# Kernel optimization log

Hardware: AMD Instinct MI355X
Metric: run time of the kernel (lower is better)

Reference implementation:

```python
import jax, jax.numpy as jnp
import numpy as np

D_MODEL, D_STATE, D_CONV, EXPAND = 1024, 16, 4, 2
D_INNER = EXPAND * D_MODEL          # 2048
DT_RANK = D_MODEL // 16             # 64
B, L = 2, 1024


def setup_inputs() -> dict:
    key = jax.random.key(0)
    ks = jax.random.split(key, 10)
    x = jax.random.normal(ks[0], (B, L, D_MODEL), dtype=jnp.float32)
    ln_w = jnp.ones((D_MODEL,), jnp.float32)
    ln_b = jnp.zeros((D_MODEL,), jnp.float32)
    in_proj_w = jax.random.normal(ks[1], (2 * D_INNER, D_MODEL), jnp.float32) * (D_MODEL ** -0.5)
    conv_w = jax.random.normal(ks[2], (D_INNER, 1, D_CONV), jnp.float32) * (D_CONV ** -0.5)
    conv_b = jnp.zeros((D_INNER,), jnp.float32)
    x_proj_w = jax.random.normal(ks[3], (DT_RANK + 2 * D_STATE, D_INNER), jnp.float32) * (D_INNER ** -0.5)
    dt_proj_w = jax.random.normal(ks[4], (D_INNER, DT_RANK), jnp.float32) * (DT_RANK ** -0.5)
    # dt bias: inverse-softplus of dt sampled log-uniform in [1e-3, 1e-1] (mamba init)
    dt = jnp.exp(jax.random.uniform(ks[5], (D_INNER,)) * (np.log(0.1) - np.log(1e-3)) + np.log(1e-3))
    dt_proj_b = dt + jnp.log(-jnp.expm1(-dt))
    # A_log: log of [1..d_state] repeated per channel (S4D-real init)
    A_log = jnp.log(jnp.broadcast_to(jnp.arange(1, D_STATE + 1, dtype=jnp.float32), (D_INNER, D_STATE)))
    D = jnp.ones((D_INNER,), jnp.float32)
    out_proj_w = jax.random.normal(ks[6], (D_MODEL, D_INNER), jnp.float32) * (D_INNER ** -0.5)
    return dict(x=x, ln_w=ln_w, ln_b=ln_b, in_proj_w=in_proj_w, conv_w=conv_w,
                conv_b=conv_b, x_proj_w=x_proj_w, dt_proj_w=dt_proj_w,
                dt_proj_b=dt_proj_b, A_log=A_log, D=D, out_proj_w=out_proj_w)


def _layernorm(x, w, b, eps=1e-5):
    mu = jnp.mean(x, axis=-1, keepdims=True)
    var = jnp.mean(jnp.square(x - mu), axis=-1, keepdims=True)
    return (x - mu) * jax.lax.rsqrt(var + eps) * w + b


def _mamba(h, in_proj_w, conv_w, conv_b, x_proj_w, dt_proj_w, dt_proj_b, A_log, D, out_proj_w):
    # h: (B, L, d_model)
    xz = jnp.einsum('bld,ed->ble', h, in_proj_w)          # (B,L,2*d_inner)
    x_in, z = jnp.split(xz, 2, axis=-1)                   # each (B,L,d_inner)
    # depthwise causal conv1d
    kernel = jnp.transpose(conv_w, (2, 1, 0))             # (d_conv, 1, d_inner) LIO
    x_conv = jax.lax.conv_general_dilated(
        x_in, kernel, window_strides=(1,), padding=[(D_CONV - 1, 0)],
        dimension_numbers=('NLC', 'LIO', 'NLC'), feature_group_count=D_INNER)
    x_conv = jax.nn.silu(x_conv + conv_b)                 # (B,L,d_inner)
    # input-dependent SSM parameters
    x_dbl = jnp.einsum('bld,ed->ble', x_conv, x_proj_w)   # (B,L,dt_rank+2*d_state)
    dt, B_ssm, C_ssm = jnp.split(x_dbl, [DT_RANK, DT_RANK + D_STATE], axis=-1)
    dt = jax.nn.softplus(jnp.einsum('blr,dr->bld', dt, dt_proj_w) + dt_proj_b)  # (B,L,d_inner)
    A = -jnp.exp(A_log)                                   # (d_inner, d_state)
    deltaA = jnp.exp(dt[..., None] * A)                   # (B,L,d_inner,d_state)
    deltaBu = dt[..., None] * B_ssm[:, :, None, :] * x_conv[..., None]
    # selective scan: h_t = deltaA_t * h_{t-1} + deltaBu_t (parallel associative scan over L)
    def combine(left, right):
        a_l, b_l = left
        a_r, b_r = right
        return a_l * a_r, b_l * a_r + b_r
    _, states = jax.lax.associative_scan(combine, (deltaA, deltaBu), axis=1)
    y = jnp.einsum('blds,bls->bld', states, C_ssm) + x_conv * D
    y = y * jax.nn.silu(z)
    return jnp.einsum('bld,ed->ble', y, out_proj_w)       # (B,L,d_model)


def reference(x, ln_w, ln_b, in_proj_w, conv_w, conv_b, x_proj_w, dt_proj_w,
              dt_proj_b, A_log, D, out_proj_w):
    h = _layernorm(x, ln_w, ln_b)
    return x + _mamba(h, in_proj_w, conv_w, conv_b, x_proj_w, dt_proj_w,
                      dt_proj_b, A_log, D, out_proj_w)
```

## Files before the change

kernel.cpp:

```cpp
#include <hip/hip_runtime.h>
#include <hip/hip_bf16.h>
#include <math.h>

#define DM   1024
#define DI   2048
#define DS   16
#define DTR  64
#define NB   2
#define LL   1024
#define MR   (NB*LL)
#define XDBL 96
#define NC   32
#define CL   32

typedef _Float16 half8  __attribute__((ext_vector_type(8)));
typedef _Float16 half4v __attribute__((ext_vector_type(4)));
typedef float    floatx4 __attribute__((ext_vector_type(4)));

__device__ __forceinline__ void gload_lds16(const void* g, void* l) {
  __builtin_amdgcn_global_load_lds(
      (const __attribute__((address_space(1))) void*)g,
      (__attribute__((address_space(3))) void*)l, 16, 0, 0);
}

__global__ __launch_bounds__(256) void front_kernel(
    const float* __restrict__ x, const float* __restrict__ ln_w,
    const float* __restrict__ ln_b,
    const float* __restrict__ w_in, const float* __restrict__ w_out,
    const float* __restrict__ w_xp, const float* __restrict__ w_dt,
    _Float16* __restrict__ h_h,
    _Float16* __restrict__ w_in_h, _Float16* __restrict__ w_out_h,
    _Float16* __restrict__ w_xp_h, _Float16* __restrict__ w_dt_h) {
  const int blk = blockIdx.x;
  if (blk < MR) {
    __shared__ float sA[4], sB[4];
    const float* xr = x + (size_t)blk * DM;
    float s = 0.f, ss = 0.f;
    for (int i = threadIdx.x; i < DM; i += 256) {
      float v = xr[i];
      s += v; ss += v * v;
    }
    for (int o = 32; o > 0; o >>= 1) {
      s  += __shfl_down(s, o, 64);
      ss += __shfl_down(ss, o, 64);
    }
    const int wid = threadIdx.x >> 6, lid = threadIdx.x & 63;
    if (lid == 0) { sA[wid] = s; sB[wid] = ss; }
    __syncthreads();
    if (threadIdx.x == 0) {
      float S = sA[0] + sA[1] + sA[2] + sA[3];
      float SS = sB[0] + sB[1] + sB[2] + sB[3];
      float mu = S / DM;
      sA[0] = mu;
      sB[0] = rsqrtf(SS / DM - mu * mu + 1e-5f);
    }
    __syncthreads();
    const float mu = sA[0], rs = sB[0];
    for (int i = threadIdx.x; i < DM; i += 256)
      h_h[(size_t)blk * DM + i] = (_Float16)((xr[i] - mu) * rs * ln_w[i] + ln_b[i]);
    return;
  }
  int i = (blk - MR) * 256 + threadIdx.x;
  const int N0 = 1048576, N1 = 524288, N2 = 49152, N3 = 32768;
  const float* s; _Float16* d; int off;
  if (i < N0)            { s = w_in;  d = w_in_h;  off = i; }
  else if (i < N0+N1)    { s = w_out; d = w_out_h; off = i - N0; }
  else if (i < N0+N1+N2) { s = w_xp;  d = w_xp_h;  off = i - N0 - N1; }
  else if (i < N0+N1+N2+N3) { s = w_dt; d = w_dt_h; off = i - N0 - N1 - N2; }
  else return;
  float4 v = ((const float4*)s)[off];
  half4v h = {(_Float16)v.x, (_Float16)v.y, (_Float16)v.z, (_Float16)v.w};
  ((half4v*)d)[off] = h;
}

template <int EPI, int TN, int KS>
__global__ __launch_bounds__(256) void gemm_mfma(
    const _Float16* __restrict__ A,
    const _Float16* __restrict__ W,
    void* __restrict__ Cv, void* __restrict__ C2v,
    const float* __restrict__ extra, int ldc,
    int M, int N, int K, int kchunk) {
  constexpr int NT = (TN + 31) / 32;
  constexpr int WSLOT = TN / 16;
  constexpr int SLAB = 32 * KS;
  __shared__ alignas(16) _Float16 As[2][128 * 32 * KS];
  __shared__ alignas(16) _Float16 Ws[2][TN * 32 * KS];
  const int t = threadIdx.x;
  const int wave = t >> 6, lane = t & 63;
  const int m0 = blockIdx.y * 128, n0 = blockIdx.x * TN;
  const int k_beg = blockIdx.z * kchunk;
  const int nk = kchunk / SLAB;
  const int wm = (wave >> 1) * 64, wn = (wave & 1) * (TN / 2);
  floatx4 acc[4][NT];
#pragma unroll
  for (int i = 0; i < 4; i++)
#pragma unroll
    for (int j = 0; j < NT; j++) acc[i][j] = {0.f, 0.f, 0.f, 0.f};

  const int fr = lane & 15;
  const int kc8 = lane >> 4;
  const int kp = (kc8 ^ ((fr >> 1) & 3)) * 8;

  auto stage = [&](int buf, int k0) {
    for (int sl = wave; sl < 8 * KS; sl += 4) {
      const int ss = sl >> 3, s8 = sl & 7;
      const int idx = s8 * 64 + lane;
      const int row = idx >> 2;
      const int kc = (idx & 3) ^ ((row >> 1) & 3);
      gload_lds16(A + (size_t)(m0 + row) * K + k0 + ss * 32 + kc * 8,
                  &As[buf][ss * 4096 + s8 * 512]);
    }
    for (int sl = wave; sl < WSLOT * KS; sl += 4) {
      const int ss = sl / WSLOT, sw = sl % WSLOT;
      const int idx = sw * 64 + lane;
      const int row = idx >> 2;
      const int kc = (idx & 3) ^ ((row >> 1) & 3);
      const int wrow = (n0 + row < N) ? row : 0;
      gload_lds16(W + (size_t)(n0 + wrow) * K + k0 + ss * 32 + kc * 8,
                  &Ws[buf][ss * (TN * 32) + sw * 512]);
    }
  };

  stage(0, k_beg);
  int cur = 0;
  for (int ki = 0; ki < nk; ki++) {
    __syncthreads();
    if (ki + 1 < nk) stage(cur ^ 1, k_beg + (ki + 1) * SLAB);
#pragma unroll
    for (int ks = 0; ks < KS; ks++) {
      half8 af[4], wf[NT];
#pragma unroll
      for (int i = 0; i < 4; i++)
        af[i] = *(const half8*)&As[cur][ks * 4096 + (wm + i * 16 + fr) * 32 + kp];
#pragma unroll
      for (int j = 0; j < NT; j++)
        wf[j] = *(const half8*)&Ws[cur][ks * (TN * 32) + (wn + j * 16 + fr) * 32 + kp];
#pragma unroll
      for (int i = 0; i < 4; i++)
#pragma unroll
        for (int j = 0; j < NT; j++)
          acc[i][j] = __builtin_amdgcn_mfma_f32_16x16x32_f16(af[i], wf[j], acc[i][j], 0, 0, 0);
    }
    cur ^= 1;
  }

  const int col = lane & 15, rowq = lane >> 4;
#pragma unroll
  for (int i = 0; i < 4; i++) {
#pragma unroll
    for (int j = 0; j < NT; j++) {
      const int n = n0 + wn + j * 16 + col;
      if (n < N) {
#pragma unroll
        for (int r = 0; r < 4; r++) {
          const int m = m0 + wm + i * 16 + rowq * 4 + r;
          float v = acc[i][j][r];
          if (EPI == 0) {
            if (n < DI) ((_Float16*)Cv )[(size_t)m * DI + n]      = (_Float16)v;
            else        ((_Float16*)C2v)[(size_t)m * DI + n - DI] = (_Float16)v;
          } else if (EPI == 4) {
            ((_Float16*)Cv)[((size_t)blockIdx.z * M + m) * ldc + n] = (_Float16)v;
          } else if (EPI == 5) {
            v += extra[n];
            v = (v > 20.f) ? v : __logf(1.f + __expf(v));
            ((_Float16*)Cv)[(size_t)m * ldc + n] = (_Float16)v;
          }
        }
      }
    }
  }
}

__global__ __launch_bounds__(256) void xproj_reduce(
    const _Float16* __restrict__ part,
    float* __restrict__ x_dbl, _Float16* __restrict__ dtr) {
  const int idx = blockIdx.x * 256 + threadIdx.x;
  const int m = idx / XDBL, c = idx - m * XDBL;
  float s = 0.f;
#pragma unroll
  for (int z = 0; z < 16; z++) s += (float)part[(size_t)z * (MR * XDBL) + idx];
  x_dbl[idx] = s;
  if (c < DTR) dtr[m * DTR + c] = (_Float16)s;
}

__global__ __launch_bounds__(256) void out_reduce(
    const float* __restrict__ x, const _Float16* __restrict__ part,
    float* __restrict__ out) {
  const int i = blockIdx.x * 256 + threadIdx.x;
  float4 a = ((const float4*)x)[i];
#pragma unroll
  for (int z = 0; z < 4; z++) {
    half4v p = ((const half4v*)(part + (size_t)z * MR * DM))[i];
    a.x += (float)p.x; a.y += (float)p.y; a.z += (float)p.z; a.w += (float)p.w;
  }
  ((float4*)out)[i] = a;
}

__global__ __launch_bounds__(256) void conv_silu_kernel(
    const _Float16* __restrict__ xin, const float* __restrict__ cw,
    const float* __restrict__ cb, _Float16* __restrict__ xc) {
  const int idx = blockIdx.x * 256 + threadIdx.x;
  const int d8 = idx & (DI / 8 - 1);
  const int ml = idx >> 8;
  const int l  = ml & (LL - 1);
  const int d0 = d8 * 8;
  half8 xr[4];
  const half8 zero = {0, 0, 0, 0, 0, 0, 0, 0};
#pragma unroll
  for (int k = 0; k < 4; k++) {
    const int lp = l - 3 + k;
    xr[k] = (lp >= 0) ? *(const half8*)&xin[(size_t)(ml - 3 + k) * DI + d0] : zero;
  }
  half8 o;
#pragma unroll
  for (int j = 0; j < 8; j++) {
    float acc = cb[d0 + j];
#pragma unroll
    for (int k = 0; k < 4; k++)
      acc += (float)xr[k][j] * cw[(d0 + j) * 4 + k];
    o[j] = (_Float16)(acc / (1.f + __expf(-acc)));
  }
  *(half8*)&xc[(size_t)ml * DI + d0] = o;
}

__device__ __forceinline__ bool load_a(const float* __restrict__ A_log, int d,
                                       float* a) {
  const float4* Ap = (const float4*)(A_log + (size_t)d * DS);
  bool fast = true;
#pragma unroll
  for (int i = 0; i < 4; i++) {
    float4 v = Ap[i];
    a[4 * i + 0] = -__expf(v.x); a[4 * i + 1] = -__expf(v.y);
    a[4 * i + 2] = -__expf(v.z); a[4 * i + 3] = -__expf(v.w);
  }
#pragma unroll
  for (int s = 0; s < DS; s++)
    fast = fast && (fabsf(a[s] + (float)(s + 1)) < 1e-4f);
  return fast;
}

__global__ __launch_bounds__(256) void scan_phase1(
    const _Float16* __restrict__ xc,
    const float* __restrict__ xdbl,
    const _Float16* __restrict__ dtm,
    const float* __restrict__ A_log,
    float* __restrict__ HE,
    float* __restrict__ SA) {
  __shared__ float Bs[CL][DS];
  const int bi = blockIdx.x;
  const int dblk = bi & 7;
  const int c = (bi >> 3) & (NC - 1);
  const int b = bi >> 8;
  const int t = threadIdx.x;
  const int d = dblk * 256 + t;
  const int mlbase = b * LL + c * CL;

  for (int i = t; i < CL * DS; i += 256) {
    int tt = i >> 4, s = i & 15;
    Bs[tt][s] = xdbl[(size_t)(mlbase + tt) * XDBL + DTR + s];
  }

  float a[DS];
  const bool fast = load_a(A_log, d, a);
  float h[DS];
#pragma unroll
  for (int s = 0; s < DS; s++) h[s] = 0.f;
  float S = 0.f;
  __syncthreads();

  if (fast) {
    for (int tt = 0; tt < CL; tt++) {
      const size_t ml = mlbase + tt;
      const float dtv = (float)dtm[ml * DI + d];
      const float u   = (float)xc[ml * DI + d];
      const float du  = dtv * u;
      S += dtv;
      const float r = __expf(-dtv);
      float P = 1.f;
#pragma unroll
      for (int s = 0; s < DS; s++) {
        P *= r;
        h[s] = P * h[s] + du * Bs[tt][s];
      }
    }
  } else {
    for (int tt = 0; tt < CL; tt++) {
      const size_t ml = mlbase + tt;
      const float dtv = (float)dtm[ml * DI + d];
      const float u   = (float)xc[ml * DI + d];
      const float du  = dtv * u;
      S += dtv;
#pragma unroll
      for (int s = 0; s < DS; s++)
        h[s] = __expf(dtv * a[s]) * h[s] + du * Bs[tt][s];
    }
  }
  const size_t base = ((size_t)(b * NC + c) * DS) * DI + d;
#pragma unroll
  for (int s = 0; s < DS; s++) HE[base + (size_t)s * DI] = h[s];
  SA[(size_t)(b * NC + c) * DI + d] = S;
}

__global__ __launch_bounds__(256) void scan_phase2(
    const float* __restrict__ A_log,
    const float* __restrict__ SA,
    float* __restrict__ HE) {
  const int idx = blockIdx.x * 256 + threadIdx.x;
  const int d = idx & (DI - 1);
  const int s = (idx >> 11) & (DS - 1);
  const int b = idx >> 15;
  const float a = -__expf(A_log[(size_t)d * DS + s]);
  float Hc = 0.f;
  for (int c = 0; c < NC; c++) {
    const size_t o = ((size_t)(b * NC + c) * DS + s) * DI + d;
    const float he = HE[o];
    const float P = __expf(a * SA[(size_t)(b * NC + c) * DI + d]);
    HE[o] = Hc;
    Hc = P * Hc + he;
  }
}

__global__ __launch_bounds__(256) void scan_phase3(
    const _Float16* __restrict__ xc,
    const float* __restrict__ xdbl,
    const _Float16* __restrict__ dtm,
    const _Float16* __restrict__ zbuf,
    const float* __restrict__ A_log,
    const float* __restrict__ Dvec,
    const float* __restrict__ HE,
    _Float16* __restrict__ y) {
  __shared__ float Bs[CL][DS];
  __shared__ float Cs[CL][DS];
  const int bi = blockIdx.x;
  const int dblk = bi & 7;
  const int c = (bi >> 3) & (NC - 1);
  const int b = bi >> 8;
  const int t = threadIdx.x;
  const int d = dblk * 256 + t;
  const int mlbase = b * LL + c * CL;

  for (int i = t; i < CL * DS; i += 256) {
    int tt = i >> 4, s = i & 15;
    const size_t ro = (size_t)(mlbase + tt) * XDBL + DTR + s;
    Bs[tt][s] = xdbl[ro];
    Cs[tt][s] = xdbl[ro + DS];
  }

  float a[DS];
  const bool fast = load_a(A_log, d, a);
  float h[DS];
  const size_t base = ((size_t)(b * NC + c) * DS) * DI + d;
#pragma unroll
  for (int s = 0; s < DS; s++) h[s] = HE[base + (size_t)s * DI];
  const float Dv = Dvec[d];
  __syncthreads();

  if (fast) {
    for (int tt = 0; tt < CL; tt++) {
      const size_t ml = mlbase + tt;
      const float dtv = (float)dtm[ml * DI + d];
      const float u   = (float)xc[ml * DI + d];
      const float du  = dtv * u;
      const float r = __expf(-dtv);
      float P = 1.f, p = 0.f;
#pragma unroll
      for (int s = 0; s < DS; s++) {
        P *= r;
        h[s] = P * h[s] + du * Bs[tt][s];
        p += h[s] * Cs[tt][s];
      }
      const float zv = (float)zbuf[ml * DI + d];
      const float sil = zv / (1.f + __expf(-zv));
      y[ml * DI + d] = (_Float16)((p + u * Dv) * sil);
    }
  } else {
    for (int tt = 0; tt < CL; tt++) {
      const size_t ml = mlbase + tt;
      const float dtv = (float)dtm[ml * DI + d];
      const float u   = (float)xc[ml * DI + d];
      const float du  = dtv * u;
      float p = 0.f;
#pragma unroll
      for (int s = 0; s < DS; s++) {
        h[s] = __expf(dtv * a[s]) * h[s] + du * Bs[tt][s];
        p += h[s] * Cs[tt][s];
      }
      const float zv = (float)zbuf[ml * DI + d];
      const float sil = zv / (1.f + __expf(-zv));
      y[ml * DI + d] = (_Float16)((p + u * Dv) * sil);
    }
  }
}

extern "C" void kernel_launch(void* const* d_in, const int* in_sizes, int n_in,
                              void* d_out, int out_size, void* d_ws, size_t ws_size,
                              hipStream_t stream) {
  const float* x         = (const float*)d_in[0];
  const float* ln_w      = (const float*)d_in[1];
  const float* ln_b      = (const float*)d_in[2];
  const float* in_proj_w = (const float*)d_in[3];
  const float* conv_w    = (const float*)d_in[4];
  const float* conv_b    = (const float*)d_in[5];
  const float* x_proj_w  = (const float*)d_in[6];
  const float* dt_proj_w = (const float*)d_in[7];
  const float* dt_proj_b = (const float*)d_in[8];
  const float* A_log     = (const float*)d_in[9];
  const float* Dvec      = (const float*)d_in[10];
  const float* out_proj_w= (const float*)d_in[11];
  float* out = (float*)d_out;

  char* ws = (char*)d_ws;
  _Float16* h_h      = (_Float16*)ws;
  _Float16* xin_h    = (_Float16*)(ws + 4194304);
  _Float16* y_h      = xin_h;
  _Float16* z_h      = (_Float16*)(ws + 12582912);
  _Float16* xc_h     = (_Float16*)(ws + 20971520);
  _Float16* dtb_h    = (_Float16*)(ws + 29360128);
  _Float16* out_part = dtb_h;
  float*    x_dbl    = (float*)   (ws + 46137344);
  float*    SA       = (float*)   (ws + 46923776);
  _Float16* dtr_h    = (_Float16*)(ws + 47448064);
  float*    HE       = (float*)   (ws + 47710208);
  _Float16* w_in_h   = (_Float16*)(ws + 56098816);
  _Float16* w_out_h  = (_Float16*)(ws + 64487424);
  _Float16* w_xp_h   = (_Float16*)(ws + 68681728);
  _Float16* w_dt_h   = (_Float16*)(ws + 69074944);
  _Float16* xp_part  = (_Float16*)(ws + 69337088);

  front_kernel<<<MR + 6464, 256, 0, stream>>>(
      x, ln_w, ln_b, in_proj_w, out_proj_w, x_proj_w, dt_proj_w,
      h_h, w_in_h, w_out_h, w_xp_h, w_dt_h);

  gemm_mfma<0, 128, 2><<<dim3(2 * DI / 128, MR / 128, 1), 256, 0, stream>>>(
      h_h, w_in_h, xin_h, z_h, nullptr, 0, MR, 2 * DI, DM, DM);

  conv_silu_kernel<<<(MR * DI / 8) / 256, 256, 0, stream>>>(xin_h, conv_w, conv_b, xc_h);

  gemm_mfma<4, 96, 2><<<dim3(1, MR / 128, 16), 256, 0, stream>>>(
      xc_h, w_xp_h, xp_part, nullptr, nullptr, XDBL, MR, XDBL, DI, DI / 16);
  xproj_reduce<<<(MR * XDBL) / 256, 256, 0, stream>>>(xp_part, x_dbl, dtr_h);

  gemm_mfma<5, 64, 2><<<dim3(DI / 64, MR / 128, 1), 256, 0, stream>>>(
      dtr_h, w_dt_h, dtb_h, nullptr, dt_proj_b, DI, MR, DI, DTR, DTR);

  scan_phase1<<<NB * NC * (DI / 256), 256, 0, stream>>>(
      xc_h, x_dbl, dtb_h, A_log, HE, SA);
  scan_phase2<<<(NB * DS * DI) / 256, 256, 0, stream>>>(A_log, SA, HE);
  scan_phase3<<<NB * NC * (DI / 256), 256, 0, stream>>>(
      xc_h, x_dbl, dtb_h, z_h, A_log, Dvec, HE, y_h);

  gemm_mfma<4, 128, 2><<<dim3(DM / 128, MR / 128, 4), 256, 0, stream>>>(
      y_h, w_out_h, out_part, nullptr, nullptr, DM, MR, DM, DI, DI / 4);
  out_reduce<<<(MR * DM / 4) / 256, 256, 0, stream>>>(x, out_part, out);
}
```

Before: 223.6 us.

## Replace double-buffered GEMM k-loop with four-buffer ring and explicit vmcnt waits

The MFMA GEMM drops its double buffer with 64-wide k slabs and moves to a four-slot LDS ring of 32-wide k slabs. Three slabs are prefetched ahead through global_load_lds, and a manual s_waitcnt vmcnt plus a raw s_barrier replaces __syncthreads. The MFMA block is wrapped in s_setprio to favour math issue. The goal is to hide global-load latency behind more in-flight stages, at the cost of twice as many barriers per K and hand-tuned wait counts that must match the per-wave load count.

```diff
diff --git a/kernel.cpp b/kernel.cpp
--- a/kernel.cpp
+++ b/kernel.cpp
@@ -73,7 +73,7 @@
   ((half4v*)d)[off] = h;
 }
 
-template <int EPI, int TN, int KS>
+template <int EPI, int TN>
 __global__ __launch_bounds__(256) void gemm_mfma(
     const _Float16* __restrict__ A,
     const _Float16* __restrict__ W,
@@ -82,14 +82,14 @@
     int M, int N, int K, int kchunk) {
   constexpr int NT = (TN + 31) / 32;
   constexpr int WSLOT = TN / 16;
-  constexpr int SLAB = 32 * KS;
-  __shared__ alignas(16) _Float16 As[2][128 * 32 * KS];
-  __shared__ alignas(16) _Float16 Ws[2][TN * 32 * KS];
+  constexpr int LPS = 2 + (WSLOT >= 8 ? 2 : 1);
+  __shared__ alignas(16) _Float16 As[4][128 * 32];
+  __shared__ alignas(16) _Float16 Ws[4][TN * 32];
   const int t = threadIdx.x;
   const int wave = t >> 6, lane = t & 63;
   const int m0 = blockIdx.y * 128, n0 = blockIdx.x * TN;
   const int k_beg = blockIdx.z * kchunk;
-  const int nk = kchunk / SLAB;
+  const int nk = kchunk / 32;
   const int wm = (wave >> 1) * 64, wn = (wave & 1) * (TN / 2);
   floatx4 acc[4][NT];
 #pragma unroll
@@ -102,46 +102,51 @@
   const int kp = (kc8 ^ ((fr >> 1) & 3)) * 8;
 
   auto stage = [&](int buf, int k0) {
-    for (int sl = wave; sl < 8 * KS; sl += 4) {
-      const int ss = sl >> 3, s8 = sl & 7;
-      const int idx = s8 * 64 + lane;
+    for (int sl = wave; sl < 8; sl += 4) {
+      const int idx = sl * 64 + lane;
       const int row = idx >> 2;
       const int kc = (idx & 3) ^ ((row >> 1) & 3);
-      gload_lds16(A + (size_t)(m0 + row) * K + k0 + ss * 32 + kc * 8,
-                  &As[buf][ss * 4096 + s8 * 512]);
-    }
-    for (int sl = wave; sl < WSLOT * KS; sl += 4) {
-      const int ss = sl / WSLOT, sw = sl % WSLOT;
-      const int idx = sw * 64 + lane;
+      gload_lds16(A + (size_t)(m0 + row) * K + k0 + kc * 8,
+                  &As[buf][sl * 512]);
+    }
+    for (int sl = wave; sl < WSLOT; sl += 4) {
+      const int idx = sl * 64 + lane;
       const int row = idx >> 2;
       const int kc = (idx & 3) ^ ((row >> 1) & 3);
       const int wrow = (n0 + row < N) ? row : 0;
-      gload_lds16(W + (size_t)(n0 + wrow) * K + k0 + ss * 32 + kc * 8,
-                  &Ws[buf][ss * (TN * 32) + sw * 512]);
+      gload_lds16(W + (size_t)(n0 + wrow) * K + k0 + kc * 8,
+                  &Ws[buf][sl * 512]);
     }
   };
 
-  stage(0, k_beg);
-  int cur = 0;
+  const int npre = nk < 3 ? nk : 3;
+  for (int p = 0; p < npre; p++) stage(p, k_beg + p * 32);
+
   for (int ki = 0; ki < nk; ki++) {
-    __syncthreads();
-    if (ki + 1 < nk) stage(cur ^ 1, k_beg + (ki + 1) * SLAB);
-#pragma unroll
-    for (int ks = 0; ks < KS; ks++) {
-      half8 af[4], wf[NT];
-#pragma unroll
-      for (int i = 0; i < 4; i++)
-        af[i] = *(const half8*)&As[cur][ks * 4096 + (wm + i * 16 + fr) * 32 + kp];
+    const int rem = nk - 1 - ki;
+    if (rem >= 2)
+      asm volatile("s_waitcnt vmcnt(%0)" :: "n"(2 * LPS) : "memory");
+    else if (rem == 1)
+      asm volatile("s_waitcnt vmcnt(%0)" :: "n"(LPS) : "memory");
+    else
+      asm volatile("s_waitcnt vmcnt(0)" ::: "memory");
+    __builtin_amdgcn_s_barrier();
+    const int cur = ki & 3;
+    half8 af[4], wf[NT];
+#pragma unroll
+    for (int i = 0; i < 4; i++)
+      af[i] = *(const half8*)&As[cur][(wm + i * 16 + fr) * 32 + kp];
+#pragma unroll
+    for (int j = 0; j < NT; j++)
+      wf[j] = *(const half8*)&Ws[cur][(wn + j * 16 + fr) * 32 + kp];
+    __builtin_amdgcn_s_setprio(1);
+#pragma unroll
+    for (int i = 0; i < 4; i++)
 #pragma unroll
       for (int j = 0; j < NT; j++)
-        wf[j] = *(const half8*)&Ws[cur][ks * (TN * 32) + (wn + j * 16 + fr) * 32 + kp];
-#pragma unroll
-      for (int i = 0; i < 4; i++)
-#pragma unroll
-        for (int j = 0; j < NT; j++)
-          acc[i][j] = __builtin_amdgcn_mfma_f32_16x16x32_f16(af[i], wf[j], acc[i][j], 0, 0, 0);
-    }
-    cur ^= 1;
+        acc[i][j] = __builtin_amdgcn_mfma_f32_16x16x32_f16(af[i], wf[j], acc[i][j], 0, 0, 0);
+    __builtin_amdgcn_s_setprio(0);
+    if (ki + 3 < nk) stage((ki + 3) & 3, k_beg + (ki + 3) * 32);
   }
 
   const int col = lane & 15, rowq = lane >> 4;
@@ -431,16 +436,16 @@
       x, ln_w, ln_b, in_proj_w, out_proj_w, x_proj_w, dt_proj_w,
       h_h, w_in_h, w_out_h, w_xp_h, w_dt_h);
 
-  gemm_mfma<0, 128, 2><<<dim3(2 * DI / 128, MR / 128, 1), 256, 0, stream>>>(
+  gemm_mfma<0, 128><<<dim3(2 * DI / 128, MR / 128, 1), 256, 0, stream>>>(
       h_h, w_in_h, xin_h, z_h, nullptr, 0, MR, 2 * DI, DM, DM);
 
   conv_silu_kernel<<<(MR * DI / 8) / 256, 256, 0, stream>>>(xin_h, conv_w, conv_b, xc_h);
 
-  gemm_mfma<4, 96, 2><<<dim3(1, MR / 128, 16), 256, 0, stream>>>(
+  gemm_mfma<4, 96><<<dim3(1, MR / 128, 16), 256, 0, stream>>>(
       xc_h, w_xp_h, xp_part, nullptr, nullptr, XDBL, MR, XDBL, DI, DI / 16);
   xproj_reduce<<<(MR * XDBL) / 256, 256, 0, stream>>>(xp_part, x_dbl, dtr_h);
 
-  gemm_mfma<5, 64, 2><<<dim3(DI / 64, MR / 128, 1), 256, 0, stream>>>(
+  gemm_mfma<5, 64><<<dim3(DI / 64, MR / 128, 1), 256, 0, stream>>>(
       dtr_h, w_dt_h, dtb_h, nullptr, dt_proj_b, DI, MR, DI, DTR, DTR);
 
   scan_phase1<<<NB * NC * (DI / 256), 256, 0, stream>>>(
@@ -449,7 +454,7 @@
   scan_phase3<<<NB * NC * (DI / 256), 256, 0, stream>>>(
       xc_h, x_dbl, dtb_h, z_h, A_log, Dvec, HE, y_h);
 
-  gemm_mfma<4, 128, 2><<<dim3(DM / 128, MR / 128, 4), 256, 0, stream>>>(
+  gemm_mfma<4, 128><<<dim3(DM / 128, MR / 128, 4), 256, 0, stream>>>(
       y_h, w_out_h, out_part, nullptr, nullptr, DM, MR, DM, DI, DI / 4);
   out_reduce<<<(MR * DM / 4) / 256, 256, 0, stream>>>(x, out_part, out);
 }
```

Result: no change. 224.8 us (+0.5%).
